# Optimization experiments

Measured on AMD Instinct MI355X. Metric: run time of the kernel, lower is better.

The kernel has to match this reference:

```python
import jax, jax.numpy as jnp
import numpy as np


def setup_inputs() -> dict:
    key = jax.random.key(0)
    k1, k2, k3, k4, k5 = jax.random.split(key, 5)
    B, N, C = 16, 1024, 768
    x = jax.random.normal(k1, (B, N, C), dtype=jnp.float32)
    sc_token = jax.random.normal(k2, (1, 196, C), dtype=jnp.float32) * 0.02  # trunc_normal std=0.02
    W_qkv = jax.random.normal(k3, (C, 3 * C), dtype=jnp.float32) * 0.02
    W_proj = jax.random.normal(k4, (C, C), dtype=jnp.float32) * 0.02
    b_proj = jax.random.normal(k5, (C,), dtype=jnp.float32) * 0.02
    return {"x": x, "sc_token": sc_token, "W_qkv": W_qkv, "W_proj": W_proj, "b_proj": b_proj}


def reference(x, sc_token, W_qkv, W_proj, b_proj):
    B, N, C = x.shape
    H = 12
    Dh = C // H
    scale = Dh ** -0.5
    # concat learnable style/content tokens: [B, N1, C]
    xt = jnp.concatenate([x, jnp.broadcast_to(sc_token, (B,) + sc_token.shape[1:])], axis=1)
    N1 = xt.shape[1]
    qkv = (xt @ W_qkv).reshape(B, N1, 3, H, Dh)
    q = qkv[:, :, 0].transpose(0, 2, 1, 3)  # [B,H,N1,Dh]
    k = qkv[:, :, 1].transpose(0, 2, 1, 3)
    v = qkv[:, :, 2].transpose(0, 2, 1, 3)
    attn = jax.nn.softmax(jnp.einsum('bhqd,bhkd->bhqk', q, k) * scale, axis=-1)
    out = jnp.einsum('bhqk,bhkd->bhqd', attn, v)  # [B,H,N1,Dh]
    out = out.transpose(0, 2, 1, 3).reshape(B, N1, C)
    out = out[:, :N, :]  # drop appended tokens
    return out @ W_proj + b_proj
```

## Files before the change

### kernel.cpp

```cpp
#include <hip/hip_runtime.h>
#include <hip/hip_bf16.h>

#define BB 16
#define NN 1024
#define CC 768
#define HH 12
#define DH 64
#define NSC 196
#define N1 1220
#define MPAD 19584
#define M_QKV (BB * N1)
#define N_QKV (3 * CC)
#define M_PROJ (BB * NN)
#define KP 1224

typedef __attribute__((ext_vector_type(8))) short short8;
typedef __attribute__((ext_vector_type(4))) float f32x4;

#define SC2F 0.125f

__device__ __forceinline__ void load_lds16(const void* g, void* l) {
    __builtin_amdgcn_global_load_lds(
        (__attribute__((address_space(1))) void*)(g),
        (__attribute__((address_space(3))) void*)(l),
        16, 0, 0);
}

__global__ __launch_bounds__(256) void cast_xt_kernel(
    const float* __restrict__ x, const float* __restrict__ sct,
    __hip_bfloat16* __restrict__ xt)
{
    const int e   = blockIdx.x * 256 + threadIdx.x;
    const int row = e / 96;
    const int c8  = (e - row * 96) * 8;
    union { short8 s; __hip_bfloat16 h[8]; } u;
    if (row < M_QKV) {
        const int b  = row / N1;
        const int rr = row - b * N1;
        const float* src = (rr < NN)
            ? x   + ((size_t)b * NN + rr) * CC + c8
            : sct + (size_t)(rr - NN) * CC + c8;
        const float4 v0 = *(const float4*)src;
        const float4 v1 = *(const float4*)(src + 4);
        u.h[0] = __float2bfloat16(v0.x); u.h[1] = __float2bfloat16(v0.y);
        u.h[2] = __float2bfloat16(v0.z); u.h[3] = __float2bfloat16(v0.w);
        u.h[4] = __float2bfloat16(v1.x); u.h[5] = __float2bfloat16(v1.y);
        u.h[6] = __float2bfloat16(v1.z); u.h[7] = __float2bfloat16(v1.w);
    } else {
#pragma unroll
        for (int j = 0; j < 8; ++j) u.h[j] = __float2bfloat16(0.f);
    }
    *(short8*)(xt + (size_t)row * CC + c8) = u.s;
}

__global__ __launch_bounds__(256) void cast_wt_kernel(
    const float* __restrict__ W, __hip_bfloat16* __restrict__ WT, int Ncols)
{
    const int e  = blockIdx.x * 256 + threadIdx.x;
    const int n  = e / 96;
    const int k8 = (e - n * 96) * 8;
    union { short8 s; __hip_bfloat16 h[8]; } u;
#pragma unroll
    for (int j = 0; j < 8; ++j)
        u.h[j] = __float2bfloat16(W[(size_t)(k8 + j) * Ncols + n]);
    *(short8*)(WT + (size_t)n * CC + k8) = u.s;
}

__global__ __launch_bounds__(256) void transpose_v_kernel(
    const __hip_bfloat16* __restrict__ qkv, __hip_bfloat16* __restrict__ vt)
{
    __shared__ short Ls[64 * 72];
    const int t  = threadIdx.x;
    const int kt = blockIdx.x, h = blockIdx.y, b = blockIdx.z;
    const __hip_bfloat16* vb = qkv + (size_t)b * N1 * N_QKV + 2 * CC + h * DH;

#pragma unroll
    for (int i = 0; i < 2; ++i) {
        const int c   = t + 256 * i;
        const int key = c >> 3;
        const int d8  = (c & 7) * 8;
        const int kg  = kt * 64 + key;
        union { short8 s; short hh[8]; } u;
        if (kg < N1) {
            u.s = *(const short8*)(vb + (size_t)kg * N_QKV + d8);
        } else {
#pragma unroll
            for (int j = 0; j < 8; ++j) u.hh[j] = 0;
        }
#pragma unroll
        for (int j = 0; j < 8; ++j) Ls[(d8 + j) * 72 + key] = u.hh[j];
    }
    __syncthreads();
    __hip_bfloat16* ob = vt + (size_t)(b * HH + h) * 64 * KP + kt * 64;
#pragma unroll
    for (int i = 0; i < 2; ++i) {
        const int c  = t + 256 * i;
        const int d  = c >> 3;
        const int k8 = (c & 7) * 8;
        if (kt * 64 + k8 < KP)
            *(short8*)(ob + (size_t)d * KP + k8) = *(const short8*)&Ls[d * 72 + k8];
    }
}

template <bool WRITE_BF16, bool QSCALE>
__global__ __launch_bounds__(256) void mfma_gemm_bt(
    const __hip_bfloat16* __restrict__ A,
    const __hip_bfloat16* __restrict__ BT,
    void* __restrict__ Cout,
    const float* __restrict__ bias,
    int lda, int K, int ldc)
{
    __shared__ __hip_bfloat16 As[128 * 64];
    __shared__ __hip_bfloat16 Bs[128 * 64];

    const int t    = threadIdx.x;
    const int lane = t & 63;
    const int l15  = lane & 15;
    const int quad = lane >> 4;
    const int w    = t >> 6;
    const int wm   = w & 1;
    const int wn   = w >> 1;
    const int swz  = l15 & 7;

    const int nwg = gridDim.x * gridDim.y;
    const int lin = blockIdx.y * gridDim.x + blockIdx.x;
    const int qq  = nwg >> 3, rr = nwg & 7;
    const int xcd = lin & 7, off = lin >> 3;
    const int sw  = ((xcd < rr) ? xcd * (qq + 1)
                                : rr * (qq + 1) + (xcd - rr) * qq) + off;
    const int n0 = (sw % gridDim.x) * 128;
    const int m0 = (sw / gridDim.x) * 128;

    const int rr0 = t >> 3;
    const int uu  = ((t & 7) ^ (rr0 & 7)) * 8;

    const __hip_bfloat16* gA = A  + (size_t)(m0 + rr0) * lda + uu;
    const __hip_bfloat16* gB = BT + (size_t)(n0 + rr0) * K   + uu;
    __hip_bfloat16* lA = As + t * 8;
    __hip_bfloat16* lB = Bs + t * 8;

    f32x4 acc[4][4];
#pragma unroll
    for (int mi = 0; mi < 4; ++mi)
#pragma unroll
        for (int ni = 0; ni < 4; ++ni) {
            acc[mi][ni][0] = 0.f; acc[mi][ni][1] = 0.f;
            acc[mi][ni][2] = 0.f; acc[mi][ni][3] = 0.f;
        }

    for (int k0 = 0; k0 < K; k0 += 64) {
        __syncthreads();
        load_lds16(gA,            lA);
        load_lds16(gA + 32 * lda, lA + 2048);
        load_lds16(gA + 64 * lda, lA + 4096);
        load_lds16(gA + 96 * lda, lA + 6144);
        load_lds16(gB,            lB);
        load_lds16(gB + 32 * K,   lB + 2048);
        load_lds16(gB + 64 * K,   lB + 4096);
        load_lds16(gB + 96 * K,   lB + 6144);
        gA += 64; gB += 64;
        __syncthreads();

#pragma unroll
        for (int ks = 0; ks < 2; ++ks) {
            short8 af[4], bf_[4];
            const int u = ((ks * 4 + quad) ^ swz) * 8;
#pragma unroll
            for (int mi = 0; mi < 4; ++mi)
                af[mi] = *(const short8*)&As[(wm * 64 + mi * 16 + l15) * 64 + u];
#pragma unroll
            for (int ni = 0; ni < 4; ++ni)
                bf_[ni] = *(const short8*)&Bs[(wn * 64 + ni * 16 + l15) * 64 + u];
#pragma unroll
            for (int mi = 0; mi < 4; ++mi)
#pragma unroll
                for (int ni = 0; ni < 4; ++ni)
                    acc[mi][ni] = __builtin_amdgcn_mfma_f32_16x16x32_bf16(
                        af[mi], bf_[ni], acc[mi][ni], 0, 0, 0);
        }
    }

#pragma unroll
    for (int mi = 0; mi < 4; ++mi) {
        const int rowb = m0 + wm * 64 + mi * 16 + quad * 4;
#pragma unroll
        for (int ni = 0; ni < 4; ++ni) {
            const int col = n0 + wn * 64 + ni * 16 + l15;
#pragma unroll
            for (int r = 0; r < 4; ++r) {
                const size_t idx = (size_t)(rowb + r) * ldc + col;
                if (WRITE_BF16) {
                    float v = acc[mi][ni][r];
                    if (QSCALE && n0 < CC) v *= SC2F;
                    ((__hip_bfloat16*)Cout)[idx] = __float2bfloat16(v);
                } else {
                    ((float*)Cout)[idx] = acc[mi][ni][r] + bias[col];
                }
            }
        }
    }
}

__global__ __launch_bounds__(256, 4) void attn_mfma_kernel(
    const __hip_bfloat16* qkv,
    const __hip_bfloat16* __restrict__ vt,
    __hip_bfloat16* ao)
{
    __shared__ __hip_bfloat16 Ks[64 * 64];
    __shared__ __hip_bfloat16 Vs[2][64 * 64];
    __shared__ short Pl[4 * 16 * 64];

    const int t    = threadIdx.x;
    const int l15  = t & 15;
    const int quad = (t >> 4) & 3;
    const int w    = t >> 6;
    const int swz  = l15 & 7;

    const int L    = blockIdx.x + 16 * (blockIdx.y + 12 * blockIdx.z);
    const int g    = L & 7, s = L >> 3;
    const int pair = g * 24 + (s >> 4);
    const int qt   = s & 15;
    const int h    = pair % 12;
    const int b    = pair / 12;

    const size_t rowbase = (size_t)b * N1;
    const __hip_bfloat16* qb  = qkv + rowbase * N_QKV + h * DH;
    const __hip_bfloat16* kb  = qkv + rowbase * N_QKV + CC + h * DH;
    const __hip_bfloat16* vtb = vt + (size_t)(b * HH + h) * 64 * KP;

    const int cA = t,       rA = cA >> 3, uA = (cA & 7) ^ (rA & 7);
    const int cB = t + 256, rB = cB >> 3, uB = (cB & 7) ^ (rB & 7);

#define KSTAGE(k0) do {                                                            \
        load_lds16(kb + (size_t)((k0) + rA) * N_QKV + uA * 8, (char*)Ks + cA * 16); \
        load_lds16(kb + (size_t)((k0) + rB) * N_QKV + uB * 8, (char*)Ks + cB * 16); \
    } while (0)
#define VSTAGE(bi, k0) do {                                                        \
        load_lds16(vtb + (size_t)rA * KP + (k0) + uA * 8, (char*)&Vs[(bi)][0] + cA * 16); \
        load_lds16(vtb + (size_t)rB * KP + (k0) + uB * 8, (char*)&Vs[(bi)][0] + cB * 16); \
    } while (0)

    short8 qf[2];
    {
        const size_t qrow = (size_t)(qt * 64 + w * 16 + l15);
#pragma unroll
        for (int ks = 0; ks < 2; ++ks)
            qf[ks] = *(const short8*)(qb + qrow * N_QKV + ks * 32 + quad * 8);
    }

    f32x4 oac[4];
#pragma unroll
    for (int dt = 0; dt < 4; ++dt) {
        oac[dt][0] = 0.f; oac[dt][1] = 0.f; oac[dt][2] = 0.f; oac[dt][3] = 0.f;
    }
    float lrun = 0.f;
    short* Pw = Pl + (w * 16) * 64;

    KSTAGE(0);
    VSTAGE(0, 0);
    __syncthreads();

    int cur = 0;
    for (int k0 = 0; k0 < N1; k0 += 64) {
        short8 kf[4][2];
#pragma unroll
        for (int mt = 0; mt < 4; ++mt)
#pragma unroll
            for (int ks = 0; ks < 2; ++ks)
                kf[mt][ks] = *(const short8*)
                    &Ks[(mt * 16 + l15) * 64 + ((4 * ks + quad) ^ swz) * 8];

        f32x4 st[4];
#pragma unroll
        for (int mt = 0; mt < 4; ++mt) {
            st[mt][0] = 0.f; st[mt][1] = 0.f; st[mt][2] = 0.f; st[mt][3] = 0.f;
        }
        __builtin_amdgcn_s_setprio(1);
#pragma unroll
        for (int ks = 0; ks < 2; ++ks)
#pragma unroll
            for (int mt = 0; mt < 4; ++mt)
                st[mt] = __builtin_amdgcn_mfma_f32_16x16x32_bf16(
                    kf[mt][ks], qf[ks], st[mt], 0, 0, 0);
        __builtin_amdgcn_s_setprio(0);

        __syncthreads();

        if (k0 + 64 < N1) {
            KSTAGE(k0 + 64);
            VSTAGE(cur ^ 1, k0 + 64);
        }

        if (k0 + 64 > N1) {
#pragma unroll
            for (int mt = 0; mt < 4; ++mt)
#pragma unroll
                for (int r = 0; r < 4; ++r)
                    if (k0 + mt * 16 + quad * 4 + r >= N1) st[mt][r] = -1e30f;
        }
        float rsum = 0.f;
#pragma unroll
        for (int mt = 0; mt < 4; ++mt)
#pragma unroll
            for (int r = 0; r < 4; ++r) {
                const float p = __expf(st[mt][r]);
                st[mt][r] = p;
                rsum += p;
            }
        rsum += __shfl_xor(rsum, 16);
        rsum += __shfl_xor(rsum, 32);
        lrun += rsum;

#pragma unroll
        for (int mt = 0; mt < 4; ++mt) {
            union { unsigned long long u; __hip_bfloat16 hh[4]; } pk;
#pragma unroll
            for (int r = 0; r < 4; ++r) pk.hh[r] = __float2bfloat16(st[mt][r]);
            const int unit = (2 * mt + (quad >> 1)) ^ swz;
            *(unsigned long long*)&Pw[l15 * 64 + unit * 8 + (quad & 1) * 4] = pk.u;
        }

        __builtin_amdgcn_s_setprio(1);
#pragma unroll
        for (int ks = 0; ks < 2; ++ks) {
            const short8 pf = *(const short8*)
                &Pw[l15 * 64 + ((4 * ks + quad) ^ swz) * 8];
#pragma unroll
            for (int dt = 0; dt < 4; ++dt) {
                const short8 vf = *(const short8*)
                    &Vs[cur][(l15 + 16 * dt) * 64 + ((4 * ks + quad) ^ swz) * 8];
                oac[dt] = __builtin_amdgcn_mfma_f32_16x16x32_bf16(pf, vf, oac[dt], 0, 0, 0);
            }
        }
        __builtin_amdgcn_s_setprio(0);

        __syncthreads();
        cur ^= 1;
    }
#undef KSTAGE
#undef VSTAGE

    const float li = 1.0f / lrun;
#pragma unroll
    for (int r = 0; r < 4; ++r) {
        const float ir = __shfl(li, quad * 4 + r);
        const int qrow = qt * 64 + w * 16 + quad * 4 + r;
        __hip_bfloat16* orow = ao + ((size_t)b * NN + qrow) * N_QKV + h * DH;
#pragma unroll
        for (int dt = 0; dt < 4; ++dt)
            orow[l15 + 16 * dt] = __float2bfloat16(oac[dt][r] * ir);
    }
}

extern "C" void kernel_launch(void* const* d_in, const int* in_sizes, int n_in,
                              void* d_out, int out_size, void* d_ws, size_t ws_size,
                              hipStream_t stream) {
    const float* x      = (const float*)d_in[0];
    const float* sct    = (const float*)d_in[1];
    const float* W_qkv  = (const float*)d_in[2];
    const float* W_proj = (const float*)d_in[3];
    const float* b_proj = (const float*)d_in[4];
    float* out = (float*)d_out;

    char* p = (char*)d_ws;
    __hip_bfloat16* xt      = (__hip_bfloat16*)p;
    __hip_bfloat16* vtg     = (__hip_bfloat16*)p;
    __hip_bfloat16* qkv     = (__hip_bfloat16*)(p + (size_t)MPAD * CC * 2);
    __hip_bfloat16* WTqkv   = (__hip_bfloat16*)(p + (size_t)MPAD * CC * 2 + (size_t)MPAD * N_QKV * 2);
    __hip_bfloat16* WTproj  = WTqkv + (size_t)N_QKV * CC;
    __hip_bfloat16* ao      = qkv + 2 * CC;

    cast_xt_kernel<<<MPAD * 96 / 256, 256, 0, stream>>>(x, sct, xt);
    cast_wt_kernel<<<N_QKV * 96 / 256, 256, 0, stream>>>(W_qkv, WTqkv, N_QKV);
    cast_wt_kernel<<<CC * 96 / 256, 256, 0, stream>>>(W_proj, WTproj, CC);

    mfma_gemm_bt<true, true><<<dim3(N_QKV / 128, MPAD / 128), 256, 0, stream>>>(
        xt, WTqkv, qkv, nullptr, CC, CC, N_QKV);
    transpose_v_kernel<<<dim3((N1 + 63) / 64, HH, BB), 256, 0, stream>>>(qkv, vtg);
    attn_mfma_kernel<<<dim3(NN / 64, HH, BB), 256, 0, stream>>>(qkv, vtg, ao);
    mfma_gemm_bt<false, false><<<dim3(CC / 128, M_PROJ / 128), 256, 0, stream>>>(
        ao, WTproj, out, b_proj, N_QKV, CC, CC);
}
```

Baseline: 347.3 us.

## Replace GEMM with 256x256-tile, 8-wave, double-buffered pipelined MFMA kernel

```diff
diff --git a/kernel.cpp b/kernel.cpp
--- a/kernel.cpp
+++ b/kernel.cpp
@@ -8,11 +8,11 @@
 #define DH 64
 #define NSC 196
 #define N1 1220
-#define MPAD 19584
+#define MPAD 19712
 #define M_QKV (BB * N1)
 #define N_QKV (3 * CC)
 #define M_PROJ (BB * NN)
-#define KP 1224
+#define KP 1232
 
 typedef __attribute__((ext_vector_type(8))) short short8;
 typedef __attribute__((ext_vector_type(4))) float f32x4;
@@ -97,29 +97,28 @@
         const int c  = t + 256 * i;
         const int d  = c >> 3;
         const int k8 = (c & 7) * 8;
-        if (kt * 64 + k8 < KP)
+        if (kt * 64 + k8 + 8 <= KP)
             *(short8*)(ob + (size_t)d * KP + k8) = *(const short8*)&Ls[d * 72 + k8];
     }
 }
 
 template <bool WRITE_BF16, bool QSCALE>
-__global__ __launch_bounds__(256) void mfma_gemm_bt(
+__global__ __launch_bounds__(512, 1) void gemm8p(
     const __hip_bfloat16* __restrict__ A,
     const __hip_bfloat16* __restrict__ BT,
     void* __restrict__ Cout,
     const float* __restrict__ bias,
-    int lda, int K, int ldc)
+    int lda, int K, int ldc, int Mvalid)
 {
-    __shared__ __hip_bfloat16 As[128 * 64];
-    __shared__ __hip_bfloat16 Bs[128 * 64];
+    __shared__ __hip_bfloat16 As[2 * 2 * 128 * 64];
+    __shared__ __hip_bfloat16 Bs[2 * 2 * 128 * 64];
 
     const int t    = threadIdx.x;
-    const int lane = t & 63;
-    const int l15  = lane & 15;
-    const int quad = lane >> 4;
+    const int l15  = t & 15;
+    const int quad = (t >> 4) & 3;
     const int w    = t >> 6;
-    const int wm   = w & 1;
-    const int wn   = w >> 1;
+    const int wm   = w >> 2;
+    const int wn   = w & 3;
     const int swz  = l15 & 7;
 
     const int nwg = gridDim.x * gridDim.y;
@@ -128,73 +127,113 @@
     const int xcd = lin & 7, off = lin >> 3;
     const int sw  = ((xcd < rr) ? xcd * (qq + 1)
                                 : rr * (qq + 1) + (xcd - rr) * qq) + off;
-    const int n0 = (sw % gridDim.x) * 128;
-    const int m0 = (sw / gridDim.x) * 128;
-
-    const int rr0 = t >> 3;
-    const int uu  = ((t & 7) ^ (rr0 & 7)) * 8;
-
-    const __hip_bfloat16* gA = A  + (size_t)(m0 + rr0) * lda + uu;
-    const __hip_bfloat16* gB = BT + (size_t)(n0 + rr0) * K   + uu;
-    __hip_bfloat16* lA = As + t * 8;
-    __hip_bfloat16* lB = Bs + t * 8;
-
-    f32x4 acc[4][4];
-#pragma unroll
-    for (int mi = 0; mi < 4; ++mi)
+    const int n0 = (sw % gridDim.x) * 256;
+    const int m0 = (sw / gridDim.x) * 256;
+
+    const int r0 = t >> 3;
+    const int su = ((t & 7) ^ (r0 & 7)) * 8;
+
+    const __hip_bfloat16* gA = A  + (size_t)(m0 + r0) * lda + su;
+    const __hip_bfloat16* gB = BT + (size_t)(n0 + r0) * K   + su;
+
+#define SA(kt_, half_) do {                                                     \
+        __hip_bfloat16* _l = As + (((kt_) & 1) * 2 + (half_)) * 8192 + t * 8;   \
+        const __hip_bfloat16* _g = gA + (size_t)((half_) * 128) * lda + (kt_) * 64; \
+        load_lds16(_g, _l);                                                     \
+        load_lds16(_g + (size_t)64 * lda, _l + 4096);                           \
+    } while (0)
+#define SB(kt_, half_) do {                                                     \
+        __hip_bfloat16* _l = Bs + (((kt_) & 1) * 2 + (half_)) * 8192 + t * 8;   \
+        const __hip_bfloat16* _g = gB + (size_t)((half_) * 128) * K + (kt_) * 64; \
+        load_lds16(_g, _l);                                                     \
+        load_lds16(_g + (size_t)64 * K, _l + 4096);                             \
+    } while (0)
+
+    f32x4 acc[8][4];
+#pragma unroll
+    for (int mi = 0; mi < 8; ++mi)
 #pragma unroll
         for (int ni = 0; ni < 4; ++ni) {
             acc[mi][ni][0] = 0.f; acc[mi][ni][1] = 0.f;
             acc[mi][ni][2] = 0.f; acc[mi][ni][3] = 0.f;
         }
 
-    for (int k0 = 0; k0 < K; k0 += 64) {
-        __syncthreads();
-        load_lds16(gA,            lA);
-        load_lds16(gA + 32 * lda, lA + 2048);
-        load_lds16(gA + 64 * lda, lA + 4096);
-        load_lds16(gA + 96 * lda, lA + 6144);
-        load_lds16(gB,            lB);
-        load_lds16(gB + 32 * K,   lB + 2048);
-        load_lds16(gB + 64 * K,   lB + 4096);
-        load_lds16(gB + 96 * K,   lB + 6144);
-        gA += 64; gB += 64;
-        __syncthreads();
-
-#pragma unroll
-        for (int ks = 0; ks < 2; ++ks) {
-            short8 af[4], bf_[4];
-            const int u = ((ks * 4 + quad) ^ swz) * 8;
-#pragma unroll
-            for (int mi = 0; mi < 4; ++mi)
-                af[mi] = *(const short8*)&As[(wm * 64 + mi * 16 + l15) * 64 + u];
-#pragma unroll
-            for (int ni = 0; ni < 4; ++ni)
-                bf_[ni] = *(const short8*)&Bs[(wn * 64 + ni * 16 + l15) * 64 + u];
-#pragma unroll
-            for (int mi = 0; mi < 4; ++mi)
+    SA(0, 0); SA(0, 1); SB(0, 0); SB(0, 1); SB(1, 0); SB(1, 1);
+    asm volatile("s_waitcnt vmcnt(4)" ::: "memory");
+    __builtin_amdgcn_s_barrier();
+    __builtin_amdgcn_sched_barrier(0);
+
+    const int NT = K >> 6;
+    const int brow = (wn & 1) * 64;
+    for (int kt = 0; kt < NT; ++kt) {
+        const int d = kt & 1;
+        const __hip_bfloat16* Ab = As + (d * 2 + wm) * 8192;
+        const __hip_bfloat16* Bb = Bs + (d * 2 + (wn >> 1)) * 8192;
+        short8 bf[4][2];
+
+#pragma unroll
+        for (int q = 0; q < 4; ++q) {
+            short8 af[2][2];
+#pragma unroll
+            for (int dmi = 0; dmi < 2; ++dmi)
+#pragma unroll
+                for (int ks = 0; ks < 2; ++ks)
+                    af[dmi][ks] = *(const short8*)
+                        &Ab[(q * 32 + dmi * 16 + l15) * 64 + (((ks * 4 + quad) ^ swz) << 3)];
+            if (q == 0) {
 #pragma unroll
                 for (int ni = 0; ni < 4; ++ni)
-                    acc[mi][ni] = __builtin_amdgcn_mfma_f32_16x16x32_bf16(
-                        af[mi], bf_[ni], acc[mi][ni], 0, 0, 0);
-        }
-    }
-
-#pragma unroll
-    for (int mi = 0; mi < 4; ++mi) {
-        const int rowb = m0 + wm * 64 + mi * 16 + quad * 4;
+#pragma unroll
+                    for (int ks = 0; ks < 2; ++ks)
+                        bf[ni][ks] = *(const short8*)
+                            &Bb[(brow + ni * 16 + l15) * 64 + (((ks * 4 + quad) ^ swz) << 3)];
+            }
+            if (q == 0 && kt + 1 < NT) SA(kt + 1, 0);
+            if (q == 1 && kt + 1 < NT) SA(kt + 1, 1);
+            if (q == 2 && kt + 2 < NT) SB(kt + 2, 0);
+            if (q == 3 && kt + 2 < NT) SB(kt + 2, 1);
+
+            __builtin_amdgcn_s_barrier();
+            __builtin_amdgcn_sched_barrier(0);
+            __builtin_amdgcn_s_setprio(1);
+#pragma unroll
+            for (int ks = 0; ks < 2; ++ks)
+#pragma unroll
+                for (int dmi = 0; dmi < 2; ++dmi)
+#pragma unroll
+                    for (int ni = 0; ni < 4; ++ni)
+                        acc[q * 2 + dmi][ni] = __builtin_amdgcn_mfma_f32_16x16x32_bf16(
+                            af[dmi][ks], bf[ni][ks], acc[q * 2 + dmi][ni], 0, 0, 0);
+            __builtin_amdgcn_s_setprio(0);
+
+            if (q == 3) {
+                if (kt + 2 < NT)      asm volatile("s_waitcnt vmcnt(4)" ::: "memory");
+                else if (kt + 1 < NT) asm volatile("s_waitcnt vmcnt(0)" ::: "memory");
+            }
+            __builtin_amdgcn_s_barrier();
+            __builtin_amdgcn_sched_barrier(0);
+        }
+    }
+#undef SA
+#undef SB
+
+#pragma unroll
+    for (int mi = 0; mi < 8; ++mi) {
+        const int rowb = m0 + wm * 128 + mi * 16 + quad * 4;
 #pragma unroll
         for (int ni = 0; ni < 4; ++ni) {
             const int col = n0 + wn * 64 + ni * 16 + l15;
 #pragma unroll
             for (int r = 0; r < 4; ++r) {
-                const size_t idx = (size_t)(rowb + r) * ldc + col;
-                if (WRITE_BF16) {
+                const int row = rowb + r;
+                if (row < Mvalid) {
                     float v = acc[mi][ni][r];
-                    if (QSCALE && n0 < CC) v *= SC2F;
-                    ((__hip_bfloat16*)Cout)[idx] = __float2bfloat16(v);
-                } else {
-                    ((float*)Cout)[idx] = acc[mi][ni][r] + bias[col];
+                    if (WRITE_BF16) {
+                        if (QSCALE && n0 < CC) v *= SC2F;
+                        ((__hip_bfloat16*)Cout)[(size_t)row * ldc + col] = __float2bfloat16(v);
+                    } else {
+                        ((float*)Cout)[(size_t)row * ldc + col] = v + bias[col];
+                    }
                 }
             }
         }
@@ -366,7 +405,7 @@
     __hip_bfloat16* xt      = (__hip_bfloat16*)p;
     __hip_bfloat16* vtg     = (__hip_bfloat16*)p;
     __hip_bfloat16* qkv     = (__hip_bfloat16*)(p + (size_t)MPAD * CC * 2);
-    __hip_bfloat16* WTqkv   = (__hip_bfloat16*)(p + (size_t)MPAD * CC * 2 + (size_t)MPAD * N_QKV * 2);
+    __hip_bfloat16* WTqkv   = (__hip_bfloat16*)(p + (size_t)MPAD * CC * 2 + (size_t)M_QKV * N_QKV * 2);
     __hip_bfloat16* WTproj  = WTqkv + (size_t)N_QKV * CC;
     __hip_bfloat16* ao      = qkv + 2 * CC;
 
@@ -374,10 +413,10 @@
     cast_wt_kernel<<<N_QKV * 96 / 256, 256, 0, stream>>>(W_qkv, WTqkv, N_QKV);
     cast_wt_kernel<<<CC * 96 / 256, 256, 0, stream>>>(W_proj, WTproj, CC);
 
-    mfma_gemm_bt<true, true><<<dim3(N_QKV / 128, MPAD / 128), 256, 0, stream>>>(
-        xt, WTqkv, qkv, nullptr, CC, CC, N_QKV);
+    gemm8p<true, true><<<dim3(N_QKV / 256, MPAD / 256), 512, 0, stream>>>(
+        xt, WTqkv, qkv, nullptr, CC, CC, N_QKV, M_QKV);
     transpose_v_kernel<<<dim3((N1 + 63) / 64, HH, BB), 256, 0, stream>>>(qkv, vtg);
     attn_mfma_kernel<<<dim3(NN / 64, HH, BB), 256, 0, stream>>>(qkv, vtg, ao);
-    mfma_gemm_bt<false, false><<<dim3(CC / 128, M_PROJ / 128), 256, 0, stream>>>(
-        ao, WTproj, out, b_proj, N_QKV, CC, CC);
-}
+    gemm8p<false, false><<<dim3(CC / 256, M_PROJ / 256), 512, 0, stream>>>(
+        ao, WTproj, out, b_proj, N_QKV, CC, CC, M_PROJ);
+}
```

Result: slower. 354.3 us (+2.0%).

## Double attention query tile to 128 rows with 512 threads; merge cast kernels

Applied to the files above, without the earlier changes.

```diff
diff --git a/kernel.cpp b/kernel.cpp
--- a/kernel.cpp
+++ b/kernel.cpp
@@ -14,6 +14,10 @@
 #define M_PROJ (BB * NN)
 #define KP 1224
 
+#define XT_BLOCKS (MPAD * 96 / 256)
+#define WQ_BLOCKS (N_QKV * 96 / 256)
+#define WP_BLOCKS (CC * 96 / 256)
+
 typedef __attribute__((ext_vector_type(8))) short short8;
 typedef __attribute__((ext_vector_type(4))) float f32x4;
 
@@ -26,44 +30,53 @@
         16, 0, 0);
 }
 
-__global__ __launch_bounds__(256) void cast_xt_kernel(
+__global__ __launch_bounds__(256) void cast_all_kernel(
     const float* __restrict__ x, const float* __restrict__ sct,
-    __hip_bfloat16* __restrict__ xt)
+    const float* __restrict__ W_qkv, const float* __restrict__ W_proj,
+    __hip_bfloat16* __restrict__ xt,
+    __hip_bfloat16* __restrict__ WTqkv, __hip_bfloat16* __restrict__ WTproj)
 {
-    const int e   = blockIdx.x * 256 + threadIdx.x;
-    const int row = e / 96;
-    const int c8  = (e - row * 96) * 8;
-    union { short8 s; __hip_bfloat16 h[8]; } u;
-    if (row < M_QKV) {
-        const int b  = row / N1;
-        const int rr = row - b * N1;
-        const float* src = (rr < NN)
-            ? x   + ((size_t)b * NN + rr) * CC + c8
-            : sct + (size_t)(rr - NN) * CC + c8;
-        const float4 v0 = *(const float4*)src;
-        const float4 v1 = *(const float4*)(src + 4);
-        u.h[0] = __float2bfloat16(v0.x); u.h[1] = __float2bfloat16(v0.y);
-        u.h[2] = __float2bfloat16(v0.z); u.h[3] = __float2bfloat16(v0.w);
-        u.h[4] = __float2bfloat16(v1.x); u.h[5] = __float2bfloat16(v1.y);
-        u.h[6] = __float2bfloat16(v1.z); u.h[7] = __float2bfloat16(v1.w);
+    const int blk = blockIdx.x;
+    if (blk < XT_BLOCKS) {
+        const int e   = blk * 256 + threadIdx.x;
+        const int row = e / 96;
+        const int c8  = (e - row * 96) * 8;
+        union { short8 s; __hip_bfloat16 h[8]; } u;
+        if (row < M_QKV) {
+            const int b  = row / N1;
+            const int rr = row - b * N1;
+            const float* src = (rr < NN)
+                ? x   + ((size_t)b * NN + rr) * CC + c8
+                : sct + (size_t)(rr - NN) * CC + c8;
+            const float4 v0 = *(const float4*)src;
+            const float4 v1 = *(const float4*)(src + 4);
+            u.h[0] = __float2bfloat16(v0.x); u.h[1] = __float2bfloat16(v0.y);
+            u.h[2] = __float2bfloat16(v0.z); u.h[3] = __float2bfloat16(v0.w);
+            u.h[4] = __float2bfloat16(v1.x); u.h[5] = __float2bfloat16(v1.y);
+            u.h[6] = __float2bfloat16(v1.z); u.h[7] = __float2bfloat16(v1.w);
+        } else {
+#pragma unroll
+            for (int j = 0; j < 8; ++j) u.h[j] = __float2bfloat16(0.f);
+        }
+        *(short8*)(xt + (size_t)row * CC + c8) = u.s;
     } else {
-#pragma unroll
-        for (int j = 0; j < 8; ++j) u.h[j] = __float2bfloat16(0.f);
-    }
-    *(short8*)(xt + (size_t)row * CC + c8) = u.s;
-}
-
-__global__ __launch_bounds__(256) void cast_wt_kernel(
-    const float* __restrict__ W, __hip_bfloat16* __restrict__ WT, int Ncols)
-{
-    const int e  = blockIdx.x * 256 + threadIdx.x;
-    const int n  = e / 96;
-    const int k8 = (e - n * 96) * 8;
-    union { short8 s; __hip_bfloat16 h[8]; } u;
-#pragma unroll
-    for (int j = 0; j < 8; ++j)
-        u.h[j] = __float2bfloat16(W[(size_t)(k8 + j) * Ncols + n]);
-    *(short8*)(WT + (size_t)n * CC + k8) = u.s;
+        const float* W;
+        __hip_bfloat16* WT;
+        int base, Ncols;
+        if (blk < XT_BLOCKS + WQ_BLOCKS) {
+            W = W_qkv; WT = WTqkv; base = blk - XT_BLOCKS; Ncols = N_QKV;
+        } else {
+            W = W_proj; WT = WTproj; base = blk - XT_BLOCKS - WQ_BLOCKS; Ncols = CC;
+        }
+        const int e  = base * 256 + threadIdx.x;
+        const int n  = e / 96;
+        const int k8 = (e - n * 96) * 8;
+        union { short8 s; __hip_bfloat16 h[8]; } u;
+#pragma unroll
+        for (int j = 0; j < 8; ++j)
+            u.h[j] = __float2bfloat16(W[(size_t)(k8 + j) * Ncols + n]);
+        *(short8*)(WT + (size_t)n * CC + k8) = u.s;
+    }
 }
 
 __global__ __launch_bounds__(256) void transpose_v_kernel(
@@ -201,14 +214,14 @@
     }
 }
 
-__global__ __launch_bounds__(256, 4) void attn_mfma_kernel(
+__global__ __launch_bounds__(512, 4) void attn_mfma_kernel(
     const __hip_bfloat16* qkv,
     const __hip_bfloat16* __restrict__ vt,
     __hip_bfloat16* ao)
 {
     __shared__ __hip_bfloat16 Ks[64 * 64];
     __shared__ __hip_bfloat16 Vs[2][64 * 64];
-    __shared__ short Pl[4 * 16 * 64];
+    __shared__ short Pl[8 * 16 * 64];
 
     const int t    = threadIdx.x;
     const int l15  = t & 15;
@@ -216,10 +229,10 @@
     const int w    = t >> 6;
     const int swz  = l15 & 7;
 
-    const int L    = blockIdx.x + 16 * (blockIdx.y + 12 * blockIdx.z);
+    const int L    = blockIdx.x + 8 * (blockIdx.y + 12 * blockIdx.z);
     const int g    = L & 7, s = L >> 3;
-    const int pair = g * 24 + (s >> 4);
-    const int qt   = s & 15;
+    const int pair = g * 24 + (s >> 3);
+    const int qt   = s & 7;
     const int h    = pair % 12;
     const int b    = pair / 12;
 
@@ -228,21 +241,16 @@
     const __hip_bfloat16* kb  = qkv + rowbase * N_QKV + CC + h * DH;
     const __hip_bfloat16* vtb = vt + (size_t)(b * HH + h) * 64 * KP;
 
-    const int cA = t,       rA = cA >> 3, uA = (cA & 7) ^ (rA & 7);
-    const int cB = t + 256, rB = cB >> 3, uB = (cB & 7) ^ (rB & 7);
-
-#define KSTAGE(k0) do {                                                            \
-        load_lds16(kb + (size_t)((k0) + rA) * N_QKV + uA * 8, (char*)Ks + cA * 16); \
-        load_lds16(kb + (size_t)((k0) + rB) * N_QKV + uB * 8, (char*)Ks + cB * 16); \
-    } while (0)
-#define VSTAGE(bi, k0) do {                                                        \
-        load_lds16(vtb + (size_t)rA * KP + (k0) + uA * 8, (char*)&Vs[(bi)][0] + cA * 16); \
-        load_lds16(vtb + (size_t)rB * KP + (k0) + uB * 8, (char*)&Vs[(bi)][0] + cB * 16); \
-    } while (0)
+    const int rA = t >> 3, uA = (t & 7) ^ (rA & 7);
+
+#define KSTAGE(k0) \
+    load_lds16(kb + (size_t)((k0) + rA) * N_QKV + uA * 8, (char*)Ks + t * 16)
+#define VSTAGE(bi, k0) \
+    load_lds16(vtb + (size_t)rA * KP + (k0) + uA * 8, (char*)&Vs[(bi)][0] + t * 16)
 
     short8 qf[2];
     {
-        const size_t qrow = (size_t)(qt * 64 + w * 16 + l15);
+        const size_t qrow = (size_t)(qt * 128 + w * 16 + l15);
 #pragma unroll
         for (int ks = 0; ks < 2; ++ks)
             qf[ks] = *(const short8*)(qb + qrow * N_QKV + ks * 32 + quad * 8);
@@ -344,7 +352,7 @@
 #pragma unroll
     for (int r = 0; r < 4; ++r) {
         const float ir = __shfl(li, quad * 4 + r);
-        const int qrow = qt * 64 + w * 16 + quad * 4 + r;
+        const int qrow = qt * 128 + w * 16 + quad * 4 + r;
         __hip_bfloat16* orow = ao + ((size_t)b * NN + qrow) * N_QKV + h * DH;
 #pragma unroll
         for (int dt = 0; dt < 4; ++dt)
@@ -370,14 +378,13 @@
     __hip_bfloat16* WTproj  = WTqkv + (size_t)N_QKV * CC;
     __hip_bfloat16* ao      = qkv + 2 * CC;
 
-    cast_xt_kernel<<<MPAD * 96 / 256, 256, 0, stream>>>(x, sct, xt);
-    cast_wt_kernel<<<N_QKV * 96 / 256, 256, 0, stream>>>(W_qkv, WTqkv, N_QKV);
-    cast_wt_kernel<<<CC * 96 / 256, 256, 0, stream>>>(W_proj, WTproj, CC);
+    cast_all_kernel<<<XT_BLOCKS + WQ_BLOCKS + WP_BLOCKS, 256, 0, stream>>>(
+        x, sct, W_qkv, W_proj, xt, WTqkv, WTproj);
 
     mfma_gemm_bt<true, true><<<dim3(N_QKV / 128, MPAD / 128), 256, 0, stream>>>(
         xt, WTqkv, qkv, nullptr, CC, CC, N_QKV);
     transpose_v_kernel<<<dim3((N1 + 63) / 64, HH, BB), 256, 0, stream>>>(qkv, vtg);
-    attn_mfma_kernel<<<dim3(NN / 64, HH, BB), 256, 0, stream>>>(qkv, vtg, ao);
+    attn_mfma_kernel<<<dim3(NN / 128, HH, BB), 512, 0, stream>>>(qkv, vtg, ao);
     mfma_gemm_bt<false, false><<<dim3(CC / 128, M_PROJ / 128), 256, 0, stream>>>(
         ao, WTproj, out, b_proj, N_QKV, CC, CC);
 }
```

Measured after the change: 339.4 us. 2.3% less time.
